# Kernel tuning notes

Hardware: AMD Instinct MI355X
Metric: run time of the kernel (lower is better)

Reference implementation:

```python
import jax, jax.numpy as jnp
import numpy as np
from jax import lax


def setup_inputs() -> dict:
    key = jax.random.key(0)
    ks = jax.random.split(key, 16)
    def rn(k, shape, s=0.05):
        return (jax.random.normal(k, shape) * s).astype(jnp.float32)
    B, N, F = 16, 1024, 200
    return dict(
        x=jax.random.normal(ks[0], (B, 1, N, F), dtype=jnp.float32),
        gat_W=rn(ks[1], (F, F)), att_src=rn(ks[2], (F,)), att_dst=rn(ks[3], (F,)), gat_b=rn(ks[4], (F,)),
        conv1_w=rn(ks[5], (40, 1, 1, 26)), conv1_b=rn(ks[6], (40,)),
        bn1_g=jnp.ones((40,), jnp.float32), bn1_b=jnp.zeros((40,), jnp.float32),
        bn1_m=jnp.zeros((40,), jnp.float32), bn1_v=jnp.ones((40,), jnp.float32),
        conv2_w=rn(ks[7], (40, 40, N), 0.01), conv2_b=rn(ks[8], (40,)),
        bn2_g=jnp.ones((40,), jnp.float32), bn2_b=jnp.zeros((40,), jnp.float32),
        bn2_m=jnp.zeros((40,), jnp.float32), bn2_v=jnp.ones((40,), jnp.float32),
        projc_w=rn(ks[9], (40, 40)), projc_b=rn(ks[10], (40,)),
        W1=rn(ks[11], (1400, 1024)), b1=rn(ks[12], (1024,)),
        W2=rn(ks[13], (1024, 1024)), b2=rn(ks[14], (1024,)),
        ln_g=jnp.ones((1024,), jnp.float32), ln_b=jnp.zeros((1024,), jnp.float32),
    )


def _bn(y, g, b, m, v, eps=1e-5):
    # eval-mode BatchNorm over channel axis 1
    shp = (1, -1) + (1,) * (y.ndim - 2)
    return (y - m.reshape(shp)) * (g.reshape(shp) / jnp.sqrt(v.reshape(shp) + eps)) + b.reshape(shp)


def reference(x, gat_W, att_src, att_dst, gat_b, conv1_w, conv1_b,
              bn1_g, bn1_b, bn1_m, bn1_v, conv2_w, conv2_b,
              bn2_g, bn2_b, bn2_m, bn2_v, projc_w, projc_b,
              W1, b1, W2, b2, ln_g, ln_b):
    B, _, N, F = x.shape  # (16,1,1024,200)
    # --- EEG_GAT (PyG GATConv, heads=1). edge_index only covers nodes 0..N-1;
    # add_self_loops applies to all B*N nodes -> first graph is dense attention
    # (complete graph incl. self), remaining nodes see only their self-loop.
    h = x.reshape(B * N, F) @ gat_W               # (B*N, 200)
    a_s = h[:N] @ att_src                          # source scores, first graph
    a_d = h[:N] @ att_dst                          # target scores
    logits = jax.nn.leaky_relu(a_s[None, :] + a_d[:, None], 0.2)  # [target i, source j]
    out0 = jax.nn.softmax(logits, axis=1) @ h[:N]  # (N, 200)
    gat = (jnp.concatenate([out0, h[N:]], axis=0) + gat_b).reshape(B, 1, N, F)
    x = x + gat  # ResidualAdd (dropout in eval = identity)
    # --- PatchEmbedding shallownet
    y = lax.conv_general_dilated(x, conv1_w, (1, 1), 'VALID',
                                 dimension_numbers=('NCHW', 'OIHW', 'NCHW'))
    y = y + conv1_b[None, :, None, None]           # (B,40,1024,175)
    y = y.reshape(B, 40, N, 35, 5).mean(-1)        # AvgPool2d (1,5) stride (1,5)
    y = jax.nn.elu(_bn(y, bn1_g, bn1_b, bn1_m, bn1_v))
    y = jnp.einsum('bchw,och->bow', y, conv2_w) + conv2_b[None, :, None]  # Conv2d(40,40,(1024,1)) -> (B,40,35)
    y = jax.nn.elu(_bn(y, bn2_g, bn2_b, bn2_m, bn2_v))
    # projection 1x1 conv then rearrange 'b e h w -> b (h w) e' then flatten
    y = jnp.einsum('bow,eo->bew', y, projc_w) + projc_b[None, :, None]
    y = y.transpose(0, 2, 1).reshape(B, -1)        # (B, 1400)
    # --- Proj_eeg
    z = y @ W1 + b1
    z = z + (jax.nn.gelu(z, approximate=False) @ W2 + b2)
    mu = z.mean(-1, keepdims=True)
    var = ((z - mu) ** 2).mean(-1, keepdims=True)
    return (z - mu) / jnp.sqrt(var + 1e-5) * ln_g + ln_b
```

## Files before the change

kernel.cpp:

```cpp
#include <hip/hip_runtime.h>
#include <math.h>

typedef __attribute__((ext_vector_type(8))) short short8;
typedef __attribute__((ext_vector_type(4))) float f32x4;

__device__ __forceinline__ unsigned f2bf(float f) {
  unsigned u = __float_as_uint(f);
  return (u + 0x7FFFu + ((u >> 16) & 1u)) >> 16;
}
__device__ __forceinline__ unsigned pk2(float lo, float hi) {
  return f2bf(lo) | (f2bf(hi) << 16);
}

#define WS_X1    0
#define WS_W2P   3328000
#define WS_AS    4966400
#define WS_AD    4967424
#define WS_WEFB  4968464
#define WS_S1    4969664
#define WS_SH1   4969704
#define WS_S2    4969744
#define WS_SH2   4969784
#define WS_H     4970496
#define WS_P     5232640
#define WS_AP    6281216
#define WS_Y3P   WS_P
#define WS_Y4    8378368
#define WS_Y5    8400768
#define WS_ZP    8455936
#define WS_Z2P   8570624
#define WS_WPT   8701696

__global__ __launch_bounds__(256) void k0_prep(const float* __restrict__ gat_W,
                        const float* __restrict__ conv1_w, const float* __restrict__ conv1_b,
                        const float* __restrict__ bn1_g, const float* __restrict__ bn1_b,
                        const float* __restrict__ bn1_m, const float* __restrict__ bn1_v,
                        const float* __restrict__ conv2_b,
                        const float* __restrict__ bn2_g, const float* __restrict__ bn2_b,
                        const float* __restrict__ bn2_m, const float* __restrict__ bn2_v,
                        const float* __restrict__ w2,
                        float* __restrict__ ws) {
  int bx = blockIdx.x, t = threadIdx.x;
  if (bx < 224) {
    unsigned short* wpt = (unsigned short*)(ws + WS_WPT);
    int idx = bx * 256 + t;
    int n = idx / 224, k = idx % 224;
    float v = (n < 200 && k < 200) ? gat_W[k * 200 + n] : 0.f;
    wpt[idx] = (unsigned short)f2bf(v);
    return;
  }
  if (bx == 224) {
    if (t < 48) {
      unsigned short* wb = (unsigned short*)(ws + WS_WEFB);
      float wv[30];
      if (t < 40) {
        for (int j = 0; j < 30; ++j) {
          float s = 0.f;
          for (int tt = 0; tt < 5; ++tt) {
            int k = j - tt;
            if (k >= 0 && k < 26) s += conv1_w[t * 26 + k];
          }
          wv[j] = s * 0.2f;
        }
      }
      for (int k = 0; k < 32; ++k)
        wb[t * 32 + k] = (unsigned short)f2bf((t < 40 && k < 30) ? wv[k] : 0.f);
    }
    if (t < 40) {
      float s1 = bn1_g[t] * rsqrtf(bn1_v[t] + 1e-5f);
      ws[WS_S1 + t] = s1;
      ws[WS_SH1 + t] = bn1_b[t] + (conv1_b[t] - bn1_m[t]) * s1;
      float s2 = bn2_g[t] * rsqrtf(bn2_v[t] + 1e-5f);
      ws[WS_S2 + t] = s2;
      ws[WS_SH2 + t] = bn2_b[t] + (conv2_b[t] - bn2_m[t]) * s2;
    }
    return;
  }
  __shared__ unsigned short lds[2560];
  int q = bx - 225;
  int c8 = q / 6, o0 = (q % 6) * 8;
  unsigned short* w2p = (unsigned short*)(ws + WS_W2P);
#pragma unroll
  for (int i = 0; i < 10; ++i) {
    int e = i * 256 + t;
    int o = e / 320, rr = e % 320;
    int c = rr / 8, nl = rr % 8;
    int oa = o0 + o;
    float v = (oa < 40) ? w2[(oa * 40 + c) * 1024 + c8 * 8 + nl] : 0.f;
    lds[o * 320 + nl * 40 + c] = (unsigned short)f2bf(v);
  }
  __syncthreads();
  uint4* src = (uint4*)lds;
  uint4* dst = (uint4*)(w2p + (c8 * 48 + o0) * 320);
  for (int i = t; i < 320; i += 256) dst[i] = src[i];
}

__global__ __launch_bounds__(256) void k1_mfma(const float* __restrict__ x,
                                               const unsigned short* __restrict__ wpt,
                                               const float* __restrict__ gat_b,
                                               float* __restrict__ h,
                                               float* __restrict__ x1) {
  __shared__ unsigned short Bt[64 * 232];
  __shared__ unsigned short As[2][64 * 40];
  int t = threadIdx.x;
  int wave = t >> 6, lane = t & 63;
  int m16 = lane & 15, quad = lane >> 4;
  int row0 = blockIdx.x * 64, n0 = blockIdx.y * 64;
  for (int i = t; i < 1792; i += 256) {
    int row = i / 28, ch = i % 28;
    *(short8*)&Bt[row * 232 + ch * 8] = *(const short8*)&wpt[(n0 + row) * 224 + ch * 8];
  }
  {
    int m = t >> 2, kq = (t & 3) * 8;
    const float* xr = x + (row0 + m) * 200 + kq;
    float4 a = *(const float4*)xr;
    float4 b = *(const float4*)(xr + 4);
    uint4 pv;
    pv.x = pk2(a.x, a.y); pv.y = pk2(a.z, a.w);
    pv.z = pk2(b.x, b.y); pv.w = pk2(b.z, b.w);
    *(uint4*)&As[0][m * 40 + kq] = pv;
  }
  __syncthreads();
  f32x4 acc0 = {0.f, 0.f, 0.f, 0.f}, acc1 = acc0, acc2 = acc0, acc3 = acc0;
  int buf = 0;
  for (int s = 0; s < 7; ++s) {
    if (s < 6) {
      int m = t >> 2, kq = (t & 3) * 8;
      int kg = (s + 1) * 32 + kq;
      const float* xr = x + (row0 + m) * 200;
      uint4 pv;
      if (kg + 8 <= 200) {
        float4 a = *(const float4*)(xr + kg);
        float4 b = *(const float4*)(xr + kg + 4);
        pv.x = pk2(a.x, a.y); pv.y = pk2(a.z, a.w);
        pv.z = pk2(b.x, b.y); pv.w = pk2(b.z, b.w);
      } else {
        float e[8];
#pragma unroll
        for (int q = 0; q < 8; ++q) e[q] = (kg + q < 200) ? xr[kg + q] : 0.f;
        pv.x = pk2(e[0], e[1]); pv.y = pk2(e[2], e[3]);
        pv.z = pk2(e[4], e[5]); pv.w = pk2(e[6], e[7]);
      }
      *(uint4*)&As[buf ^ 1][m * 40 + kq] = pv;
    }
    short8 af = *(const short8*)&As[buf][(wave * 16 + m16) * 40 + quad * 8];
    int kb = s * 32 + quad * 8;
    short8 b0 = *(const short8*)&Bt[(0 * 16 + m16) * 232 + kb];
    short8 b1 = *(const short8*)&Bt[(1 * 16 + m16) * 232 + kb];
    short8 b2 = *(const short8*)&Bt[(2 * 16 + m16) * 232 + kb];
    short8 b3 = *(const short8*)&Bt[(3 * 16 + m16) * 232 + kb];
    acc0 = __builtin_amdgcn_mfma_f32_16x16x32_bf16(af, b0, acc0, 0, 0, 0);
    acc1 = __builtin_amdgcn_mfma_f32_16x16x32_bf16(af, b1, acc1, 0, 0, 0);
    acc2 = __builtin_amdgcn_mfma_f32_16x16x32_bf16(af, b2, acc2, 0, 0, 0);
    acc3 = __builtin_amdgcn_mfma_f32_16x16x32_bf16(af, b3, acc3, 0, 0, 0);
    __syncthreads();
    buf ^= 1;
  }
  f32x4 accs[4] = {acc0, acc1, acc2, acc3};
  if (blockIdx.x < 16) {
#pragma unroll
    for (int nt = 0; nt < 4; ++nt)
#pragma unroll
      for (int r = 0; r < 4; ++r) {
        int row = row0 + wave * 16 + quad * 4 + r;
        h[row * 256 + n0 + nt * 16 + m16] = accs[nt][r];
      }
  } else {
#pragma unroll
    for (int nt = 0; nt < 4; ++nt) {
      int col = n0 + nt * 16 + m16;
      if (col < 200) {
#pragma unroll
        for (int r = 0; r < 4; ++r) {
          int row = row0 + wave * 16 + quad * 4 + r;
          x1[row * 200 + col] = x[row * 200 + col] + accs[nt][r] + gat_b[col];
        }
      }
    }
  }
}

__global__ __launch_bounds__(256) void k1b_scores(const float* __restrict__ h,
                                                  const float* __restrict__ att_src,
                                                  const float* __restrict__ att_dst,
                                                  float* __restrict__ as_,
                                                  float* __restrict__ ad_) {
  int t = threadIdx.x;
  int wave = t >> 6, lane = t & 63;
  int r = blockIdx.x * 4 + wave;
  float s = 0.f, d = 0.f;
  if (lane < 50) {
    float4 v = *(const float4*)(h + r * 256 + lane * 4);
    float4 a = *(const float4*)(att_src + lane * 4);
    float4 dd = *(const float4*)(att_dst + lane * 4);
    s = v.x * a.x + v.y * a.y + v.z * a.z + v.w * a.w;
    d = v.x * dd.x + v.y * dd.y + v.z * dd.z + v.w * dd.w;
  }
#pragma unroll
  for (int off = 32; off > 0; off >>= 1) {
    s += __shfl_down(s, off);
    d += __shfl_down(d, off);
  }
  if (lane == 0) {
    as_[r] = s;
    ad_[r] = d;
  }
}

__global__ __launch_bounds__(256) void kP(const float* __restrict__ as_,
                                          const float* __restrict__ ad_,
                                          float* __restrict__ P) {
  __shared__ float rb[256];
  int t = threadIdx.x, i = blockIdx.x;
  float a0 = as_[t], a1 = as_[256 + t], a2 = as_[512 + t], a3 = as_[768 + t];
  rb[t] = fmaxf(fmaxf(a0, a1), fmaxf(a2, a3));
  __syncthreads();
  for (int st = 128; st > 0; st >>= 1) {
    if (t < st) rb[t] = fmaxf(rb[t], rb[t + st]);
    __syncthreads();
  }
  float maxs = rb[0];
  __syncthreads();
  float ad = ad_[i];
  float mv = maxs + ad;
  float M = mv >= 0.f ? mv : 0.2f * mv;
  float av[4] = {a0, a1, a2, a3};
  float p[4];
  float s = 0.f;
#pragma unroll
  for (int q = 0; q < 4; ++q) {
    float v = av[q] + ad;
    float l = v >= 0.f ? v : 0.2f * v;
    p[q] = __expf(l - M);
    s += p[q];
  }
  rb[t] = s;
  __syncthreads();
  for (int st = 128; st > 0; st >>= 1) {
    if (t < st) rb[t] += rb[t + st];
    __syncthreads();
  }
  float inv = 1.f / rb[0];
#pragma unroll
  for (int q = 0; q < 4; ++q) P[i * 1024 + q * 256 + t] = p[q] * inv;
}

__global__ __launch_bounds__(256) void kAttn(const float* __restrict__ P,
                                             const float* __restrict__ h,
                                             float* __restrict__ ap) {
  __shared__ __align__(16) float As2[8][64];
  __shared__ __align__(16) float Bs[8][64];
  int t = threadIdx.x;
  int tm = t & 15, tn = t >> 4;
  int i0 = blockIdx.x * 64, f0 = blockIdx.y * 64, j0 = blockIdx.z * 128;
  float acc[4][4] = {};
  for (int k0 = 0; k0 < 128; k0 += 8) {
    for (int i = t; i < 512; i += 256) {
      int m = i >> 3, k = i & 7;
      As2[k][m] = P[(i0 + m) * 1024 + j0 + k0 + k];
    }
    for (int i = t; i < 512; i += 256) {
      int k = i >> 6, n = i & 63;
      Bs[k][n] = h[(j0 + k0 + k) * 256 + f0 + n];
    }
    __syncthreads();
#pragma unroll
    for (int k = 0; k < 8; ++k) {
      float4 a = *(const float4*)&As2[k][tm * 4];
      float4 bq = *(const float4*)&Bs[k][tn * 4];
      float av[4] = {a.x, a.y, a.z, a.w};
      float bv[4] = {bq.x, bq.y, bq.z, bq.w};
#pragma unroll
      for (int i = 0; i < 4; ++i)
#pragma unroll
        for (int j = 0; j < 4; ++j) acc[i][j] += av[i] * bv[j];
    }
    __syncthreads();
  }
#pragma unroll
  for (int i = 0; i < 4; ++i) {
    int r = i0 + tm * 4 + i;
    float4 v = make_float4(acc[i][0], acc[i][1], acc[i][2], acc[i][3]);
    *(float4*)&ap[(blockIdx.z * 1024 + r) * 256 + f0 + tn * 4] = v;
  }
}

__global__ __launch_bounds__(256) void kAttnRed(const float* __restrict__ ap,
                                                const float* __restrict__ x,
                                                const float* __restrict__ gat_b,
                                                float* __restrict__ x1) {
  int t = threadIdx.x, r = blockIdx.x;
  if (t >= 200) return;
  float s = 0.f;
#pragma unroll
  for (int z = 0; z < 8; ++z) s += ap[(z * 1024 + r) * 256 + t];
  x1[r * 200 + t] = x[r * 200 + t] + s + gat_b[t];
}

__global__ __launch_bounds__(320, 2) void k3_conv(const float* __restrict__ x1,
                                                  const unsigned short* __restrict__ w2pre,
                                                  const unsigned short* __restrict__ weffB,
                                                  const float* __restrict__ ws,
                                                  float* __restrict__ y3p) {
  __shared__ __align__(16) char smem[48448];
  float* xbp = (float*)smem;
  unsigned short* tA = (unsigned short*)(smem + 6400);
  unsigned short* t2 = (unsigned short*)(smem + 24832);
  int t = threadIdx.x;
  int b = blockIdx.x, nc = blockIdx.y;
  int n0 = nc * 8;
  int wave = t >> 6, lane = t & 63;
  int l15 = lane & 15, quad = lane >> 4;
  for (int i = t; i < 400; i += 320) {
    int nn = i / 50, q = i % 50;
    ((float4*)(xbp + nn * 200))[q] = ((const float4*)(x1 + (b * 1024 + n0 + nn) * 200))[q];
  }
  __syncthreads();
  if (t < 280) {
    int nn = t / 35, p = t % 35;
    const float* xr = xbp + nn * 200 + p * 5;
    uint pv[16];
#pragma unroll
    for (int kk = 0; kk < 15; ++kk) pv[kk] = pk2(xr[kk * 2], xr[kk * 2 + 1]);
    pv[15] = 0u;
    uint4* dst = (uint4*)(tA + t * 32);
    dst[0] = make_uint4(pv[0], pv[1], pv[2], pv[3]);
    dst[1] = make_uint4(pv[4], pv[5], pv[6], pv[7]);
    dst[2] = make_uint4(pv[8], pv[9], pv[10], pv[11]);
    dst[3] = make_uint4(pv[12], pv[13], pv[14], pv[15]);
  } else if (t < 288) {
    uint4 z = make_uint4(0u, 0u, 0u, 0u);
    uint4* dst = (uint4*)(tA + t * 32);
    dst[0] = z; dst[1] = z; dst[2] = z; dst[3] = z;
  }
  __syncthreads();
  {
    int mt0 = wave * 4;
    int nmt = wave < 4 ? 4 : 2;
    short8 bw[3];
    float s1v[3] = {0.f, 0.f, 0.f}, sh1v[3] = {0.f, 0.f, 0.f};
#pragma unroll
    for (int nt = 0; nt < 3; ++nt) {
      bw[nt] = *(const short8*)&weffB[(nt * 16 + l15) * 32 + quad * 8];
      int c = nt * 16 + l15;
      if (c < 40) {
        s1v[nt] = ws[WS_S1 + c];
        sh1v[nt] = ws[WS_SH1 + c];
      }
    }
    for (int mi = 0; mi < nmt; ++mi) {
      int mt = mt0 + mi;
      short8 a = *(const short8*)&tA[(mt * 16 + l15) * 32 + quad * 8];
#pragma unroll
      for (int nt = 0; nt < 3; ++nt) {
        int c = nt * 16 + l15;
        if (c >= 40) continue;
        f32x4 c4 = {0.f, 0.f, 0.f, 0.f};
        c4 = __builtin_amdgcn_mfma_f32_16x16x32_bf16(a, bw[nt], c4, 0, 0, 0);
#pragma unroll
        for (int r = 0; r < 4; ++r) {
          int m = mt * 16 + quad * 4 + r;
          if (m < 280) {
            float v = c4[r] * s1v[nt] + sh1v[nt];
            float e = v > 0.f ? v : __expf(v) - 1.f;
            int p = m % 35, nn = m / 35;
            t2[p * 328 + nn * 40 + c] = (unsigned short)f2bf(e);
          }
        }
      }
    }
  }
  __syncthreads();
  f32x4 acc[3][3];
#pragma unroll
  for (int mt = 0; mt < 3; ++mt)
#pragma unroll
    for (int nt = 0; nt < 3; ++nt) acc[mt][nt] = (f32x4){0.f, 0.f, 0.f, 0.f};
  const unsigned short* bbase = w2pre + nc * 48 * 320;
#pragma unroll
  for (int ks = 0; ks < 2; ++ks) {
    int koff = wave * 64 + ks * 32 + quad * 8;
    short8 a[3], bb[3];
#pragma unroll
    for (int mt = 0; mt < 3; ++mt) {
      int row = mt * 16 + l15;
      row = row > 35 ? 35 : row;
      a[mt] = *(const short8*)&t2[row * 328 + koff];
    }
#pragma unroll
    for (int nt = 0; nt < 3; ++nt)
      bb[nt] = *(const short8*)&bbase[(nt * 16 + l15) * 320 + koff];
#pragma unroll
    for (int mt = 0; mt < 3; ++mt)
#pragma unroll
      for (int nt = 0; nt < 3; ++nt)
        acc[mt][nt] = __builtin_amdgcn_mfma_f32_16x16x32_bf16(a[mt], bb[nt], acc[mt][nt], 0, 0, 0);
  }
  __syncthreads();
  float* red0 = (float*)smem;
  float* red1 = red0 + 48 * 49;
  if (wave < 2) {
    float* r = wave ? red1 : red0;
#pragma unroll
    for (int mt = 0; mt < 3; ++mt)
#pragma unroll
      for (int nt = 0; nt < 3; ++nt)
#pragma unroll
        for (int q = 0; q < 4; ++q)
          r[(mt * 16 + quad * 4 + q) * 49 + nt * 16 + l15] = acc[mt][nt][q];
  }
  __syncthreads();
  if (wave == 2 || wave == 3) {
    float* r = (wave == 3) ? red1 : red0;
#pragma unroll
    for (int mt = 0; mt < 3; ++mt)
#pragma unroll
      for (int nt = 0; nt < 3; ++nt)
#pragma unroll
        for (int q = 0; q < 4; ++q)
          r[(mt * 16 + quad * 4 + q) * 49 + nt * 16 + l15] += acc[mt][nt][q];
  }
  __syncthreads();
  if (wave == 4) {
#pragma unroll
    for (int mt = 0; mt < 3; ++mt)
#pragma unroll
      for (int nt = 0; nt < 3; ++nt)
#pragma unroll
        for (int q = 0; q < 4; ++q)
          red0[(mt * 16 + quad * 4 + q) * 49 + nt * 16 + l15] += acc[mt][nt][q];
  }
  __syncthreads();
  float* dst = y3p + (b * 128 + nc) * 1400;
  for (int idx = t; idx < 1400; idx += 320) {
    int o = idx / 35, p = idx % 35;
    dst[idx] = red0[p * 49 + o] + red1[p * 49 + o];
  }
}

__global__ __launch_bounds__(256) void k4a_red(const float* __restrict__ y3p,
                                               const float* __restrict__ ws,
                                               float* __restrict__ y4) {
  int t = threadIdx.x;
  if (t >= 200) return;
  int b = blockIdx.x;
  int idx = blockIdx.y * 200 + t;
  float s = 0.f;
#pragma unroll 4
  for (int q = 0; q < 128; ++q) s += y3p[(b * 128 + q) * 1400 + idx];
  int o = idx / 35;
  float v = s * ws[WS_S2 + o] + ws[WS_SH2 + o];
  y4[b * 1400 + idx] = v > 0.f ? v : __expf(v) - 1.f;
}

__global__ __launch_bounds__(256) void k4b_proj(const float* __restrict__ y4,
                                                const float* __restrict__ projc_w,
                                                const float* __restrict__ projc_b,
                                                float* __restrict__ y5) {
  __shared__ __align__(16) float tls[1400];
  int t = threadIdx.x, b = blockIdx.x;
  for (int i = t; i < 350; i += 256)
    ((float4*)tls)[i] = ((const float4*)(y4 + b * 1400))[i];
  __syncthreads();
  for (int idx = t; idx < 1400; idx += 256) {
    int p = idx / 40, e = idx % 40;
    float acc = projc_b[e];
    for (int o = 0; o < 40; ++o) acc += tls[o * 35 + p] * projc_w[e * 40 + o];
    y5[b * 1400 + idx] = acc;
  }
}

__global__ __launch_bounds__(256) void k5_fc1(const float* __restrict__ y5,
                                              const float* __restrict__ W1,
                                              float* __restrict__ zp) {
  __shared__ __align__(16) float yls[3200];
  int t = threadIdx.x;
  int nc = blockIdx.x, kc = blockIdx.y;
  for (int i = t; i < 800; i += 256) {
    int bb = i / 50, q = i % 50;
    ((float4*)yls)[bb * 50 + q] = *(const float4*)(y5 + bb * 1400 + kc * 200 + q * 4);
  }
  __syncthreads();
  int nl = t & 31, bg = t >> 5;
  int n = nc * 32 + nl;
  float acc0 = 0.f, acc1 = 0.f;
  const float* y0 = yls + (bg * 2) * 200;
  const float* y1 = yls + (bg * 2 + 1) * 200;
  for (int k = 0; k < 200; ++k) {
    float w = W1[(kc * 200 + k) * 1024 + n];
    acc0 += y0[k] * w;
    acc1 += y1[k] * w;
  }
  zp[(kc * 16 + bg * 2) * 1024 + n] = acc0;
  zp[(kc * 16 + bg * 2 + 1) * 1024 + n] = acc1;
}

__global__ __launch_bounds__(256) void k6_fc2(const float* __restrict__ zp,
                                              const float* __restrict__ b1,
                                              const float* __restrict__ W2,
                                              float* __restrict__ z2p) {
  __shared__ __align__(16) float gls[2048];
  int t = threadIdx.x;
  int nc = blockIdx.x, kc = blockIdx.y;
  for (int i = t; i < 2048; i += 256) {
    int bb = i >> 7, kk = i & 127;
    int np = kc * 128 + kk;
    float s = b1[np];
#pragma unroll
    for (int j = 0; j < 7; ++j) s += zp[(j * 16 + bb) * 1024 + np];
    gls[i] = 0.5f * s * (1.f + erff(s * 0.70710678f));
  }
  __syncthreads();
  int nl = t & 31, bg = t >> 5;
  int n = nc * 32 + nl;
  float acc0 = 0.f, acc1 = 0.f;
  const float* g0 = gls + (bg * 2) * 128;
  const float* g1 = gls + (bg * 2 + 1) * 128;
  for (int k = 0; k < 128; ++k) {
    float w = W2[(kc * 128 + k) * 1024 + n];
    acc0 += g0[k] * w;
    acc1 += g1[k] * w;
  }
  z2p[(kc * 16 + bg * 2) * 1024 + n] = acc0;
  z2p[(kc * 16 + bg * 2 + 1) * 1024 + n] = acc1;
}

__global__ __launch_bounds__(256) void k7_ln(const float* __restrict__ zp,
                                             const float* __restrict__ z2p,
                                             const float* __restrict__ b1,
                                             const float* __restrict__ b2,
                                             const float* __restrict__ ln_g,
                                             const float* __restrict__ ln_b,
                                             float* __restrict__ out) {
  __shared__ float r1[256], r2[256];
  int t = threadIdx.x, b = blockIdx.x;
  float4 v = *(const float4*)(b1 + t * 4);
  float4 bb2 = *(const float4*)(b2 + t * 4);
  v.x += bb2.x; v.y += bb2.y; v.z += bb2.z; v.w += bb2.w;
#pragma unroll
  for (int kc = 0; kc < 7; ++kc) {
    float4 p = *(const float4*)(zp + (kc * 16 + b) * 1024 + t * 4);
    v.x += p.x; v.y += p.y; v.z += p.z; v.w += p.w;
  }
#pragma unroll
  for (int kc = 0; kc < 8; ++kc) {
    float4 p = *(const float4*)(z2p + (kc * 16 + b) * 1024 + t * 4);
    v.x += p.x; v.y += p.y; v.z += p.z; v.w += p.w;
  }
  r1[t] = v.x + v.y + v.z + v.w;
  r2[t] = v.x * v.x + v.y * v.y + v.z * v.z + v.w * v.w;
  __syncthreads();
  for (int s = 128; s > 0; s >>= 1) {
    if (t < s) {
      r1[t] += r1[t + s];
      r2[t] += r2[t + s];
    }
    __syncthreads();
  }
  float mu = r1[0] * (1.f / 1024.f);
  float var = r2[0] * (1.f / 1024.f) - mu * mu;
  float rstd = rsqrtf(var + 1e-5f);
  float4 gg = *(const float4*)(ln_g + t * 4);
  float4 bb = *(const float4*)(ln_b + t * 4);
  float4 o;
  o.x = (v.x - mu) * rstd * gg.x + bb.x;
  o.y = (v.y - mu) * rstd * gg.y + bb.y;
  o.z = (v.z - mu) * rstd * gg.z + bb.z;
  o.w = (v.w - mu) * rstd * gg.w + bb.w;
  *(float4*)(out + b * 1024 + t * 4) = o;
}

extern "C" void kernel_launch(void* const* d_in, const int* in_sizes, int n_in,
                              void* d_out, int out_size, void* d_ws, size_t ws_size,
                              hipStream_t stream) {
  (void)in_sizes; (void)n_in; (void)out_size; (void)ws_size;
  const float* x       = (const float*)d_in[0];
  const float* gat_W   = (const float*)d_in[1];
  const float* att_src = (const float*)d_in[2];
  const float* att_dst = (const float*)d_in[3];
  const float* gat_b   = (const float*)d_in[4];
  const float* conv1_w = (const float*)d_in[5];
  const float* conv2_w = (const float*)d_in[11];
  const float* projc_w = (const float*)d_in[17];
  const float* projc_b = (const float*)d_in[18];
  const float* W1      = (const float*)d_in[19];
  const float* b1      = (const float*)d_in[20];
  const float* W2      = (const float*)d_in[21];
  const float* b2      = (const float*)d_in[22];
  const float* ln_g    = (const float*)d_in[23];
  const float* ln_b    = (const float*)d_in[24];
  float* ws  = (float*)d_ws;
  float* out = (float*)d_out;

  hipLaunchKernelGGL(k0_prep, dim3(993), dim3(256), 0, stream, gat_W, conv1_w,
                     (const float*)d_in[6], (const float*)d_in[7], (const float*)d_in[8],
                     (const float*)d_in[9], (const float*)d_in[10], (const float*)d_in[12],
                     (const float*)d_in[13], (const float*)d_in[14], (const float*)d_in[15],
                     (const float*)d_in[16], conv2_w, ws);
  hipLaunchKernelGGL(k1_mfma, dim3(256, 4), dim3(256), 0, stream, x,
                     (const unsigned short*)(ws + WS_WPT), gat_b, ws + WS_H, ws + WS_X1);
  hipLaunchKernelGGL(k1b_scores, dim3(256), dim3(256), 0, stream, ws + WS_H, att_src, att_dst,
                     ws + WS_AS, ws + WS_AD);
  hipLaunchKernelGGL(kP, dim3(1024), dim3(256), 0, stream, ws + WS_AS, ws + WS_AD, ws + WS_P);
  hipLaunchKernelGGL(kAttn, dim3(16, 4, 8), dim3(256), 0, stream, ws + WS_P, ws + WS_H,
                     ws + WS_AP);
  hipLaunchKernelGGL(kAttnRed, dim3(1024), dim3(256), 0, stream, ws + WS_AP, x, gat_b,
                     ws + WS_X1);
  hipLaunchKernelGGL(k3_conv, dim3(16, 128), dim3(320), 0, stream, ws + WS_X1,
                     (const unsigned short*)(ws + WS_W2P),
                     (const unsigned short*)(ws + WS_WEFB), ws, ws + WS_Y3P);
  hipLaunchKernelGGL(k4a_red, dim3(16, 7), dim3(256), 0, stream, ws + WS_Y3P, ws, ws + WS_Y4);
  hipLaunchKernelGGL(k4b_proj, dim3(16), dim3(256), 0, stream, ws + WS_Y4, projc_w, projc_b,
                     ws + WS_Y5);
  hipLaunchKernelGGL(k5_fc1, dim3(32, 7), dim3(256), 0, stream, ws + WS_Y5, W1, ws + WS_ZP);
  hipLaunchKernelGGL(k6_fc2, dim3(32, 8), dim3(256), 0, stream, ws + WS_ZP, b1, W2,
                     ws + WS_Z2P);
  hipLaunchKernelGGL(k7_ln, dim3(16), dim3(256), 0, stream, ws + WS_ZP, ws + WS_Z2P, b1, b2,
                     ln_g, ln_b, out);
}
```

Before: 245.6 us.

## Use bf16 MFMA for attention matmul and restructure GAT projection per row-tile

The dense attention product P@h moves from a scalar fp32 FMA kernel to bf16 MFMA. P is written as bf16 and a transposed bf16 copy of h is emitted straight from the projection kernel. The projection kernel now stages each 64-row A tile once and loops over all four 64-column output chunks inside one block, which cuts A reloads and grid size. The trade-off is lower precision in the attention weights and h, plus strided transposed stores from k1.

```diff
diff --git a/kernel.cpp b/kernel.cpp
--- a/kernel.cpp
+++ b/kernel.cpp
@@ -23,6 +23,7 @@
 #define WS_SH2   4969784
 #define WS_H     4970496
 #define WS_P     5232640
+#define WS_HT    5494784
 #define WS_AP    6281216
 #define WS_Y3P   WS_P
 #define WS_Y4    8378368
@@ -99,35 +100,20 @@
                                                const unsigned short* __restrict__ wpt,
                                                const float* __restrict__ gat_b,
                                                float* __restrict__ h,
+                                               unsigned short* __restrict__ hT,
                                                float* __restrict__ x1) {
+  __shared__ unsigned short As[64 * 232];
   __shared__ unsigned short Bt[64 * 232];
-  __shared__ unsigned short As[2][64 * 40];
   int t = threadIdx.x;
   int wave = t >> 6, lane = t & 63;
   int m16 = lane & 15, quad = lane >> 4;
-  int row0 = blockIdx.x * 64, n0 = blockIdx.y * 64;
-  for (int i = t; i < 1792; i += 256) {
-    int row = i / 28, ch = i % 28;
-    *(short8*)&Bt[row * 232 + ch * 8] = *(const short8*)&wpt[(n0 + row) * 224 + ch * 8];
-  }
+  int row0 = blockIdx.x * 64;
   {
     int m = t >> 2, kq = (t & 3) * 8;
-    const float* xr = x + (row0 + m) * 200 + kq;
-    float4 a = *(const float4*)xr;
-    float4 b = *(const float4*)(xr + 4);
-    uint4 pv;
-    pv.x = pk2(a.x, a.y); pv.y = pk2(a.z, a.w);
-    pv.z = pk2(b.x, b.y); pv.w = pk2(b.z, b.w);
-    *(uint4*)&As[0][m * 40 + kq] = pv;
-  }
-  __syncthreads();
-  f32x4 acc0 = {0.f, 0.f, 0.f, 0.f}, acc1 = acc0, acc2 = acc0, acc3 = acc0;
-  int buf = 0;
-  for (int s = 0; s < 7; ++s) {
-    if (s < 6) {
-      int m = t >> 2, kq = (t & 3) * 8;
-      int kg = (s + 1) * 32 + kq;
-      const float* xr = x + (row0 + m) * 200;
+    const float* xr = x + (row0 + m) * 200;
+#pragma unroll
+    for (int s = 0; s < 7; ++s) {
+      int kg = s * 32 + kq;
       uint4 pv;
       if (kg + 8 <= 200) {
         float4 a = *(const float4*)(xr + kg);
@@ -141,42 +127,57 @@
         pv.x = pk2(e[0], e[1]); pv.y = pk2(e[2], e[3]);
         pv.z = pk2(e[4], e[5]); pv.w = pk2(e[6], e[7]);
       }
-      *(uint4*)&As[buf ^ 1][m * 40 + kq] = pv;
-    }
-    short8 af = *(const short8*)&As[buf][(wave * 16 + m16) * 40 + quad * 8];
-    int kb = s * 32 + quad * 8;
-    short8 b0 = *(const short8*)&Bt[(0 * 16 + m16) * 232 + kb];
-    short8 b1 = *(const short8*)&Bt[(1 * 16 + m16) * 232 + kb];
-    short8 b2 = *(const short8*)&Bt[(2 * 16 + m16) * 232 + kb];
-    short8 b3 = *(const short8*)&Bt[(3 * 16 + m16) * 232 + kb];
-    acc0 = __builtin_amdgcn_mfma_f32_16x16x32_bf16(af, b0, acc0, 0, 0, 0);
-    acc1 = __builtin_amdgcn_mfma_f32_16x16x32_bf16(af, b1, acc1, 0, 0, 0);
-    acc2 = __builtin_amdgcn_mfma_f32_16x16x32_bf16(af, b2, acc2, 0, 0, 0);
-    acc3 = __builtin_amdgcn_mfma_f32_16x16x32_bf16(af, b3, acc3, 0, 0, 0);
+      *(uint4*)&As[m * 232 + kg] = pv;
+    }
+  }
+  __syncthreads();
+  for (int c = 0; c < 4; ++c) {
+    int n0 = c * 64;
+    for (int i = t; i < 1792; i += 256) {
+      int row = i / 28, ch = i % 28;
+      *(short8*)&Bt[row * 232 + ch * 8] = *(const short8*)&wpt[(n0 + row) * 224 + ch * 8];
+    }
     __syncthreads();
-    buf ^= 1;
-  }
-  f32x4 accs[4] = {acc0, acc1, acc2, acc3};
-  if (blockIdx.x < 16) {
-#pragma unroll
-    for (int nt = 0; nt < 4; ++nt)
-#pragma unroll
-      for (int r = 0; r < 4; ++r) {
-        int row = row0 + wave * 16 + quad * 4 + r;
-        h[row * 256 + n0 + nt * 16 + m16] = accs[nt][r];
+    f32x4 acc[4];
+#pragma unroll
+    for (int nt = 0; nt < 4; ++nt) acc[nt] = (f32x4){0.f, 0.f, 0.f, 0.f};
+#pragma unroll
+    for (int s = 0; s < 7; ++s) {
+      short8 af = *(const short8*)&As[(wave * 16 + m16) * 232 + s * 32 + quad * 8];
+      int kb = s * 32 + quad * 8;
+#pragma unroll
+      for (int nt = 0; nt < 4; ++nt) {
+        short8 bf = *(const short8*)&Bt[(nt * 16 + m16) * 232 + kb];
+        acc[nt] = __builtin_amdgcn_mfma_f32_16x16x32_bf16(af, bf, acc[nt], 0, 0, 0);
       }
-  } else {
-#pragma unroll
-    for (int nt = 0; nt < 4; ++nt) {
-      int col = n0 + nt * 16 + m16;
-      if (col < 200) {
+    }
+    if (blockIdx.x < 16) {
+#pragma unroll
+      for (int nt = 0; nt < 4; ++nt) {
+        int col = n0 + nt * 16 + m16;
 #pragma unroll
         for (int r = 0; r < 4; ++r) {
           int row = row0 + wave * 16 + quad * 4 + r;
-          x1[row * 200 + col] = x[row * 200 + col] + accs[nt][r] + gat_b[col];
+          float v = acc[nt][r];
+          h[row * 256 + col] = v;
+          hT[col * 1024 + row] = (unsigned short)f2bf(v);
         }
       }
-    }
+    } else {
+#pragma unroll
+      for (int nt = 0; nt < 4; ++nt) {
+        int col = n0 + nt * 16 + m16;
+        if (col < 200) {
+          float gb = gat_b[col];
+#pragma unroll
+          for (int r = 0; r < 4; ++r) {
+            int row = row0 + wave * 16 + quad * 4 + r;
+            x1[row * 200 + col] = x[row * 200 + col] + acc[nt][r] + gb;
+          }
+        }
+      }
+    }
+    __syncthreads();
   }
 }
 
@@ -209,7 +210,7 @@
 
 __global__ __launch_bounds__(256) void kP(const float* __restrict__ as_,
                                           const float* __restrict__ ad_,
-                                          float* __restrict__ P) {
+                                          unsigned short* __restrict__ Pb) {
   __shared__ float rb[256];
   int t = threadIdx.x, i = blockIdx.x;
   float a0 = as_[t], a1 = as_[256 + t], a2 = as_[512 + t], a3 = as_[768 + t];
@@ -242,47 +243,38 @@
   }
   float inv = 1.f / rb[0];
 #pragma unroll
-  for (int q = 0; q < 4; ++q) P[i * 1024 + q * 256 + t] = p[q] * inv;
-}
-
-__global__ __launch_bounds__(256) void kAttn(const float* __restrict__ P,
-                                             const float* __restrict__ h,
+  for (int q = 0; q < 4; ++q)
+    Pb[i * 1024 + q * 256 + t] = (unsigned short)f2bf(p[q] * inv);
+}
+
+__global__ __launch_bounds__(256) void kAttn(const unsigned short* __restrict__ Pb,
+                                             const unsigned short* __restrict__ hT,
                                              float* __restrict__ ap) {
-  __shared__ __align__(16) float As2[8][64];
-  __shared__ __align__(16) float Bs[8][64];
   int t = threadIdx.x;
-  int tm = t & 15, tn = t >> 4;
+  int wave = t >> 6, lane = t & 63;
+  int l15 = lane & 15, quad = lane >> 4;
   int i0 = blockIdx.x * 64, f0 = blockIdx.y * 64, j0 = blockIdx.z * 128;
-  float acc[4][4] = {};
-  for (int k0 = 0; k0 < 128; k0 += 8) {
-    for (int i = t; i < 512; i += 256) {
-      int m = i >> 3, k = i & 7;
-      As2[k][m] = P[(i0 + m) * 1024 + j0 + k0 + k];
-    }
-    for (int i = t; i < 512; i += 256) {
-      int k = i >> 6, n = i & 63;
-      Bs[k][n] = h[(j0 + k0 + k) * 256 + f0 + n];
-    }
-    __syncthreads();
-#pragma unroll
-    for (int k = 0; k < 8; ++k) {
-      float4 a = *(const float4*)&As2[k][tm * 4];
-      float4 bq = *(const float4*)&Bs[k][tn * 4];
-      float av[4] = {a.x, a.y, a.z, a.w};
-      float bv[4] = {bq.x, bq.y, bq.z, bq.w};
-#pragma unroll
-      for (int i = 0; i < 4; ++i)
-#pragma unroll
-        for (int j = 0; j < 4; ++j) acc[i][j] += av[i] * bv[j];
-    }
-    __syncthreads();
-  }
-#pragma unroll
-  for (int i = 0; i < 4; ++i) {
-    int r = i0 + tm * 4 + i;
-    float4 v = make_float4(acc[i][0], acc[i][1], acc[i][2], acc[i][3]);
-    *(float4*)&ap[(blockIdx.z * 1024 + r) * 256 + f0 + tn * 4] = v;
-  }
+  int arow = i0 + wave * 16 + l15;
+  f32x4 acc[4];
+#pragma unroll
+  for (int nt = 0; nt < 4; ++nt) acc[nt] = (f32x4){0.f, 0.f, 0.f, 0.f};
+#pragma unroll
+  for (int ks = 0; ks < 4; ++ks) {
+    int koff = j0 + ks * 32 + quad * 8;
+    short8 a = *(const short8*)&Pb[arow * 1024 + koff];
+#pragma unroll
+    for (int nt = 0; nt < 4; ++nt) {
+      short8 bf = *(const short8*)&hT[(f0 + nt * 16 + l15) * 1024 + koff];
+      acc[nt] = __builtin_amdgcn_mfma_f32_16x16x32_bf16(a, bf, acc[nt], 0, 0, 0);
+    }
+  }
+#pragma unroll
+  for (int nt = 0; nt < 4; ++nt)
+#pragma unroll
+    for (int r = 0; r < 4; ++r) {
+      int row = i0 + wave * 16 + quad * 4 + r;
+      ap[(blockIdx.z * 1024 + row) * 256 + f0 + nt * 16 + l15] = acc[nt][r];
+    }
 }
 
 __global__ __launch_bounds__(256) void kAttnRed(const float* __restrict__ ap,
@@ -597,13 +589,16 @@
                      (const float*)d_in[9], (const float*)d_in[10], (const float*)d_in[12],
                      (const float*)d_in[13], (const float*)d_in[14], (const float*)d_in[15],
                      (const float*)d_in[16], conv2_w, ws);
-  hipLaunchKernelGGL(k1_mfma, dim3(256, 4), dim3(256), 0, stream, x,
-                     (const unsigned short*)(ws + WS_WPT), gat_b, ws + WS_H, ws + WS_X1);
+  hipLaunchKernelGGL(k1_mfma, dim3(256), dim3(256), 0, stream, x,
+                     (const unsigned short*)(ws + WS_WPT), gat_b, ws + WS_H,
+                     (unsigned short*)(ws + WS_HT), ws + WS_X1);
   hipLaunchKernelGGL(k1b_scores, dim3(256), dim3(256), 0, stream, ws + WS_H, att_src, att_dst,
                      ws + WS_AS, ws + WS_AD);
-  hipLaunchKernelGGL(kP, dim3(1024), dim3(256), 0, stream, ws + WS_AS, ws + WS_AD, ws + WS_P);
-  hipLaunchKernelGGL(kAttn, dim3(16, 4, 8), dim3(256), 0, stream, ws + WS_P, ws + WS_H,
-                     ws + WS_AP);
+  hipLaunchKernelGGL(kP, dim3(1024), dim3(256), 0, stream, ws + WS_AS, ws + WS_AD,
+                     (unsigned short*)(ws + WS_P));
+  hipLaunchKernelGGL(kAttn, dim3(16, 4, 8), dim3(256), 0, stream,
+                     (const unsigned short*)(ws + WS_P),
+                     (const unsigned short*)(ws + WS_HT), ws + WS_AP);
   hipLaunchKernelGGL(kAttnRed, dim3(1024), dim3(256), 0, stream, ws + WS_AP, x, gat_b,
                      ws + WS_X1);
   hipLaunchKernelGGL(k3_conv, dim3(16, 128), dim3(320), 0, stream, ws + WS_X1,
```

Measured after the change: 235.4 us. -4.2%, faster.
